# Kernel optimization log

Measured on AMD Instinct MI355X. Metric: run time of the kernel, lower is better.

Reference implementation:

```python
import jax, jax.numpy as jnp
import numpy as np
import math

B, T, C, H, RANK, RD = 8, 512, 2048, 16, 8, 16
HD = C // H  # 128
ADAPTER_SCALE = 1.0 / RANK  # scale / rank with scale=1.0


def setup_inputs() -> dict:
    key = jax.random.key(0)
    ks = jax.random.split(key, 7)
    x = jax.random.normal(ks[0], (B, T, C), dtype=jnp.float32)
    # frozen random linears (weights ~ N(0,1)/sqrt(in_features))
    Wqkv = jax.random.normal(ks[1], (3 * C, C), dtype=jnp.float32) / math.sqrt(C)
    Wout = jax.random.normal(ks[2], (C, C), dtype=jnp.float32) / math.sqrt(C)
    # VeRA frozen random matrices
    A0_qkv = jax.random.normal(ks[3], (RANK, C), dtype=jnp.float32) / math.sqrt(C)
    B0_qkv = jax.random.normal(ks[4], (3 * C, RANK), dtype=jnp.float32) / math.sqrt(RANK)
    A0_out = jax.random.normal(ks[5], (RANK, C), dtype=jnp.float32) / math.sqrt(C)
    B0_out = jax.random.normal(ks[6], (C, RANK), dtype=jnp.float32) / math.sqrt(RANK)
    # learned scaling vectors (init to ones, as in the module)
    d_a_qkv = jnp.ones((RANK,), dtype=jnp.float32)
    d_b_qkv = jnp.ones((RANK,), dtype=jnp.float32)
    d_a_out = jnp.ones((RANK,), dtype=jnp.float32)
    d_b_out = jnp.ones((RANK,), dtype=jnp.float32)
    # partial RoPE caches over first RD dims
    freqs = 1.0 / (10000.0 ** (jnp.arange(0, RD, 2, dtype=jnp.float32) / RD))  # [RD/2]
    ang = jnp.arange(T, dtype=jnp.float32)[:, None] * freqs[None, :]  # [T, RD/2]
    cos = jnp.cos(ang)
    sin = jnp.sin(ang)
    return {"x": x, "Wqkv": Wqkv, "A0_qkv": A0_qkv, "B0_qkv": B0_qkv,
            "d_a_qkv": d_a_qkv, "d_b_qkv": d_b_qkv,
            "Wout": Wout, "A0_out": A0_out, "B0_out": B0_out,
            "d_a_out": d_a_out, "d_b_out": d_b_out,
            "cos": cos, "sin": sin}


def _adapted_linear(x, W, A0, B0, d_a, d_b):
    # frozen(x) + VeRA adapter: diag(d_b) B0 diag(d_a) A0, scaled by 1/rank
    base = x @ W.T
    h = (x @ A0.T) * (d_a * d_b)
    return base + (h @ B0.T) * ADAPTER_SCALE


def _apply_rope(q, cos, sin):
    # q: [B, H, T, HD]; rotate first RD dims, pass-through the rest
    x_rope, x_pass = q[..., :RD], q[..., RD:]
    half = RD // 2
    x1, x2 = x_rope[..., :half], x_rope[..., half:]
    c = cos[None, None]  # [1,1,T,RD/2]
    s = sin[None, None]
    rot = jnp.concatenate([x1 * c - x2 * s, x2 * c + x1 * s], axis=-1)
    return jnp.concatenate([rot, x_pass], axis=-1)


def reference(x, Wqkv, A0_qkv, B0_qkv, d_a_qkv, d_b_qkv,
              Wout, A0_out, B0_out, d_a_out, d_b_out, cos, sin):
    qkv = _adapted_linear(x, Wqkv, A0_qkv, B0_qkv, d_a_qkv, d_b_qkv)  # [B,T,3C]
    qkv = qkv.reshape(B, T, 3, H, HD)
    q = jnp.transpose(qkv[:, :, 0], (0, 2, 1, 3))  # [B,H,T,HD]
    k = jnp.transpose(qkv[:, :, 1], (0, 2, 1, 3))
    v = jnp.transpose(qkv[:, :, 2], (0, 2, 1, 3))
    q = _apply_rope(q, cos, sin)
    k = _apply_rope(k, cos, sin)
    # causal SDPA
    scale = 1.0 / math.sqrt(HD)
    scores = jnp.einsum('bhqd,bhkd->bhqk', q, k) * scale
    mask = jnp.tril(jnp.ones((T, T), dtype=bool))
    scores = jnp.where(mask[None, None], scores, jnp.finfo(scores.dtype).min)
    attn = jax.nn.softmax(scores, axis=-1)
    y = jnp.einsum('bhqk,bhkd->bhqd', attn, v)  # [B,H,T,HD]
    y = jnp.transpose(y, (0, 2, 1, 3)).reshape(B, T, C)
    return _adapted_linear(y, Wout, A0_out, B0_out, d_a_out, d_b_out)
```

## Files before the change

### kernel.cpp

```cpp
#include <hip/hip_runtime.h>

typedef unsigned short ushort_t;
typedef __attribute__((ext_vector_type(8))) short short8;
typedef __attribute__((ext_vector_type(4))) float f32x4;

#define AS1(p) ((const __attribute__((address_space(1))) void*)(p))
#define AS3(p) ((__attribute__((address_space(3))) void*)(p))

__device__ __forceinline__ ushort_t f2bf(float f){
  unsigned u = __float_as_uint(f);
  u += 0x7FFFu + ((u>>16)&1u);
  return (ushort_t)(u>>16);
}
__device__ __forceinline__ float bf2f(ushort_t h){
  return __uint_as_float(((unsigned)h)<<16);
}

__global__ __launch_bounds__(256) void conv_f2b(const float* __restrict__ src,
                                                ushort_t* __restrict__ dst, int n){
  int i = (blockIdx.x*256 + threadIdx.x)*4;
  if (i < n){
    float4 v = *(const float4*)&src[i];
    ushort_t o0=f2bf(v.x), o1=f2bf(v.y), o2=f2bf(v.z), o3=f2bf(v.w);
    ushort4 o; o.x=o0; o.y=o1; o.z=o2; o.w=o3;
    *(ushort4*)&dst[i] = o;
  }
}

__global__ __launch_bounds__(256) void lora_h_f32(const float* __restrict__ X,
                                                  ushort_t* __restrict__ Xbf,
                                                  const float* __restrict__ A0,
                                                  const float* __restrict__ da,
                                                  const float* __restrict__ db,
                                                  float* __restrict__ out, int K){
  int m = blockIdx.x;
  int tid = threadIdx.x, lane = tid & 63, w = tid >> 6;
  float part[8] = {0,0,0,0,0,0,0,0};
  for (int k = tid; k < K; k += 256){
    float xv = X[(size_t)m*K + k];
    Xbf[(size_t)m*K + k] = f2bf(xv);
    #pragma unroll
    for (int r=0;r<8;++r) part[r] += xv * A0[r*K + k];
  }
  #pragma unroll
  for (int r=0;r<8;++r)
    for (int d=1;d<64;d<<=1) part[r] += __shfl_xor(part[r], d, 64);
  __shared__ float wsum[4][8];
  if (lane==0){
    #pragma unroll
    for (int r=0;r<8;++r) wsum[w][r] = part[r];
  }
  __syncthreads();
  if (tid < 8){
    float s = wsum[0][tid]+wsum[1][tid]+wsum[2][tid]+wsum[3][tid];
    out[(size_t)m*8 + tid] = s * da[tid]*db[tid];
  }
}

__global__ __launch_bounds__(256) void lora_reduce(const float* __restrict__ hpart,
                                                   const float* __restrict__ da,
                                                   const float* __restrict__ db,
                                                   float* __restrict__ out){
  int i = blockIdx.x*256 + threadIdx.x;
  int r = i & 7;
  float s = 0.f;
  #pragma unroll
  for (int hh=0; hh<16; ++hh) s += hpart[(size_t)hh*32768 + i];
  out[i] = s * da[r]*db[r];
}

__global__ __launch_bounds__(512, 1) void gemm256x192_lora(
    const ushort_t* __restrict__ A, const ushort_t* __restrict__ Bw,
    const float* __restrict__ hmat, const float* __restrict__ B0,
    ushort_t* __restrict__ C, int M, int N, int K)
{
  __shared__ __align__(16) char smem[114688];
  const int tid = threadIdx.x, lane = tid & 63, w = tid >> 6;
  const int wm = w >> 1, wn = w & 1;

  const int nbn = N / 192;
  const int nwg = (M >> 8) * nbn;
  const int q8 = nwg >> 3;
  const int swz = ((int)blockIdx.x & 7)*q8 + ((int)blockIdx.x >> 3);
  const int m0 = (swz / nbn) << 8, n0 = (swz % nbn) * 192;

  const int NTt = K >> 6;
  const int srow8  = tid >> 3;
  const int schunk = (lane & 7) ^ (lane >> 3);

  #define STAGE_AU(u, tt, bb) do { \
    const ushort_t* g_ = A + (size_t)(m0 + (u)*64 + srow8)*K + (tt)*64 + schunk*8; \
    __builtin_amdgcn_global_load_lds(AS1(g_), AS3(smem + (bb)*32768 + (u)*8192 + tid*16), 16, 0, 0); \
  } while(0)
  #define STAGE_BU(u, tt, bb) do { \
    const ushort_t* g_ = Bw + (size_t)(n0 + (u)*64 + srow8)*K + (tt)*64 + schunk*8; \
    __builtin_amdgcn_global_load_lds(AS1(g_), AS3(smem + 65536 + (bb)*24576 + (u)*8192 + tid*16), 16, 0, 0); \
  } while(0)

  #define RDA(bb, q, kk) (*(const short8*)(smem + (bb)*32768 + \
      ((q)*64 + wm*16 + (lane&15))*128 + ((((kk)*4 + (lane>>4)) ^ (lane&7))<<4)))
  #define RDB(bb, r, kk) (*(const short8*)(smem + 65536 + (bb)*24576 + \
      ((r)*32 + wn*16 + (lane&15))*128 + ((((kk)*4 + (lane>>4)) ^ (lane&7))<<4)))

  #define MM(q, r, bi) do{ \
    acc[q][r] = __builtin_amdgcn_mfma_f32_16x16x32_bf16(aF[q][0], bF[bi][0], acc[q][r], 0,0,0); \
    acc[q][r] = __builtin_amdgcn_mfma_f32_16x16x32_bf16(aF[q][1], bF[bi][1], acc[q][r], 0,0,0); \
  }while(0)

  #define BARRIER() asm volatile("s_barrier" ::: "memory")

  short8 aF[4][2];
  short8 bF[2][2];
  f32x4 acc[4][6] = {};

  STAGE_AU(0,0,0); STAGE_AU(1,0,0); STAGE_AU(2,0,0); STAGE_AU(3,0,0);
  STAGE_BU(0,0,0); STAGE_BU(1,0,0); STAGE_BU(2,0,0);
  asm volatile("s_waitcnt vmcnt(2)" ::: "memory");
  BARRIER();

  for (int t = 0; t < NTt-1; ++t){
    const int b = t & 1, nb = b ^ 1;
    #pragma unroll
    for (int q=0;q<4;++q){ aF[q][0]=RDA(b,q,0); aF[q][1]=RDA(b,q,1); }
    #pragma unroll
    for (int rl=0;rl<2;++rl){ bF[rl][0]=RDB(b,rl,0); bF[rl][1]=RDB(b,rl,1); }
    STAGE_AU(0,t+1,nb); STAGE_AU(1,t+1,nb);
    __builtin_amdgcn_s_setprio(1);
    MM(0,0,0); MM(0,1,1); MM(1,0,0); MM(1,1,1);
    MM(2,0,0); MM(2,1,1); MM(3,0,0); MM(3,1,1);
    __builtin_amdgcn_s_setprio(0);
    asm volatile("s_waitcnt vmcnt(3)" ::: "memory");
    BARRIER();
    #pragma unroll
    for (int rl=0;rl<2;++rl){ bF[rl][0]=RDB(b,rl+2,0); bF[rl][1]=RDB(b,rl+2,1); }
    STAGE_AU(2,t+1,nb); STAGE_AU(3,t+1,nb); STAGE_BU(0,t+1,nb);
    __builtin_amdgcn_s_setprio(1);
    MM(0,2,0); MM(0,3,1); MM(1,2,0); MM(1,3,1);
    MM(2,2,0); MM(2,3,1); MM(3,2,0); MM(3,3,1);
    __builtin_amdgcn_s_setprio(0);
    asm volatile("s_waitcnt vmcnt(5)" ::: "memory");
    BARRIER();
    #pragma unroll
    for (int rl=0;rl<2;++rl){ bF[rl][0]=RDB(b,rl+4,0); bF[rl][1]=RDB(b,rl+4,1); }
    STAGE_BU(1,t+1,nb); STAGE_BU(2,t+1,nb);
    __builtin_amdgcn_s_setprio(1);
    MM(0,4,0); MM(0,5,1); MM(1,4,0); MM(1,5,1);
    MM(2,4,0); MM(2,5,1); MM(3,4,0); MM(3,5,1);
    __builtin_amdgcn_s_setprio(0);
    asm volatile("s_waitcnt lgkmcnt(0)" ::: "memory");
    asm volatile("s_waitcnt vmcnt(2)" ::: "memory");
    BARRIER();
  }

  {
    const int b = (NTt-1) & 1;
    #pragma unroll
    for (int q=0;q<4;++q){ aF[q][0]=RDA(b,q,0); aF[q][1]=RDA(b,q,1); }
    #pragma unroll
    for (int rl=0;rl<2;++rl){ bF[rl][0]=RDB(b,rl,0); bF[rl][1]=RDB(b,rl,1); }
    __builtin_amdgcn_s_setprio(1);
    MM(0,0,0); MM(0,1,1); MM(1,0,0); MM(1,1,1);
    MM(2,0,0); MM(2,1,1); MM(3,0,0); MM(3,1,1);
    __builtin_amdgcn_s_setprio(0);
    asm volatile("s_waitcnt vmcnt(1)" ::: "memory");
    BARRIER();
    #pragma unroll
    for (int rl=0;rl<2;++rl){ bF[rl][0]=RDB(b,rl+2,0); bF[rl][1]=RDB(b,rl+2,1); }
    __builtin_amdgcn_s_setprio(1);
    MM(0,2,0); MM(0,3,1); MM(1,2,0); MM(1,3,1);
    MM(2,2,0); MM(2,3,1); MM(3,2,0); MM(3,3,1);
    __builtin_amdgcn_s_setprio(0);
    asm volatile("s_waitcnt vmcnt(0)" ::: "memory");
    BARRIER();
    #pragma unroll
    for (int rl=0;rl<2;++rl){ bF[rl][0]=RDB(b,rl+4,0); bF[rl][1]=RDB(b,rl+4,1); }
    MM(0,4,0); MM(0,5,1); MM(1,4,0); MM(1,5,1);
    MM(2,4,0); MM(2,5,1); MM(3,4,0); MM(3,5,1);
  }

  float b0v[6][8];
  #pragma unroll
  for (int r=0;r<6;++r){
    int col = n0 + r*32 + wn*16 + (lane&15);
    const float4* bp = (const float4*)&B0[(size_t)col*8];
    float4 u0 = bp[0], u1 = bp[1];
    b0v[r][0]=u0.x; b0v[r][1]=u0.y; b0v[r][2]=u0.z; b0v[r][3]=u0.w;
    b0v[r][4]=u1.x; b0v[r][5]=u1.y; b0v[r][6]=u1.z; b0v[r][7]=u1.w;
  }
  #pragma unroll
  for (int q=0;q<4;++q){
    #pragma unroll
    for (int jj=0;jj<4;++jj){
      int row = m0 + q*64 + wm*16 + (lane>>4)*4 + jj;
      const float4* hp = (const float4*)&hmat[(size_t)row*8];
      float4 h0 = hp[0], h1 = hp[1];
      #pragma unroll
      for (int r=0;r<6;++r){
        float lor = h0.x*b0v[r][0]+h0.y*b0v[r][1]+h0.z*b0v[r][2]+h0.w*b0v[r][3]
                  + h1.x*b0v[r][4]+h1.y*b0v[r][5]+h1.z*b0v[r][6]+h1.w*b0v[r][7];
        int col = n0 + r*32 + wn*16 + (lane&15);
        C[(size_t)row*N + col] = f2bf(acc[q][r][jj] + 0.125f*lor);
      }
    }
  }
  #undef STAGE_AU
  #undef STAGE_BU
  #undef RDA
  #undef RDB
  #undef MM
  #undef BARRIER
}

template<int MODE>
__global__ __launch_bounds__(512, 1) void gemm128x256_lora(
    const ushort_t* __restrict__ A, const ushort_t* __restrict__ Bw,
    const float* __restrict__ hmat, const float* __restrict__ B0,
    void* __restrict__ C, int M, int N, int K)
{
  __shared__ __align__(16) char smem[98304];
  const int tid = threadIdx.x, lane = tid & 63, w = tid >> 6;
  const int wm = w >> 2, wn = w & 3;

  const int nbn = N >> 8;
  const int nwg = (M >> 7) * nbn;
  const int q8 = nwg >> 3;
  const int swz = ((int)blockIdx.x & 7)*q8 + ((int)blockIdx.x >> 3);
  const int m0 = (swz / nbn) << 7, n0 = (swz % nbn) << 8;

  const int NTt = K >> 6;

  const int srow8  = tid >> 3;
  const int schunk = (lane & 7) ^ (lane >> 3);

  #define STAGE_AU(u, tt, bb) do { \
    const ushort_t* g_ = A + (size_t)(m0 + (u)*64 + srow8)*K + (tt)*64 + schunk*8; \
    __builtin_amdgcn_global_load_lds(AS1(g_), AS3(smem + (bb)*16384 + (u)*8192 + w*1024), 16, 0, 0); \
  } while(0)
  #define STAGE_BU(u, tt, bb) do { \
    const ushort_t* g_ = Bw + (size_t)(n0 + (u)*64 + srow8)*K + (tt)*64 + schunk*8; \
    __builtin_amdgcn_global_load_lds(AS1(g_), AS3(smem + 32768 + (bb)*32768 + (u)*8192 + w*1024), 16, 0, 0); \
  } while(0)

  #define RDA(bb, q, kk) (*(const short8*)(smem + (bb)*16384 + \
      ((q)*32 + wm*16 + (lane&15))*128 + ((((kk)*4 + (lane>>4)) ^ (lane&7))<<4)))
  #define RDB(bb, rg, kk) (*(const short8*)(smem + 32768 + (bb)*32768 + \
      ((rg)*64 + wn*16 + (lane&15))*128 + ((((kk)*4 + (lane>>4)) ^ (lane&7))<<4)))

  #define MM0(q,rl) do{ \
    acc[q][rl] = __builtin_amdgcn_mfma_f32_16x16x32_bf16(aF[q][0], bF[rl][0], acc[q][rl], 0,0,0); \
    acc[q][rl] = __builtin_amdgcn_mfma_f32_16x16x32_bf16(aF[q][1], bF[rl][1], acc[q][rl], 0,0,0); \
  }while(0)
  #define MM1(q,rl) do{ \
    acc[q][(rl)+2] = __builtin_amdgcn_mfma_f32_16x16x32_bf16(aF[q][0], bF[rl][0], acc[q][(rl)+2], 0,0,0); \
    acc[q][(rl)+2] = __builtin_amdgcn_mfma_f32_16x16x32_bf16(aF[q][1], bF[rl][1], acc[q][(rl)+2], 0,0,0); \
  }while(0)

  #define BARRIER() asm volatile("s_barrier" ::: "memory")

  short8 aF[4][2];
  short8 bF[2][2];
  f32x4 acc[4][4] = {};

  STAGE_AU(0,0,0); STAGE_AU(1,0,0); STAGE_BU(0,0,0); STAGE_BU(1,0,0);
  STAGE_BU(2,0,0); STAGE_BU(3,0,0);
  asm volatile("s_waitcnt vmcnt(2)" ::: "memory");
  BARRIER();

  for (int t = 0; t < NTt-1; ++t){
    const int b = t & 1, nb = b ^ 1;
    #pragma unroll
    for (int q=0;q<4;++q){ aF[q][0]=RDA(b,q,0); aF[q][1]=RDA(b,q,1); }
    #pragma unroll
    for (int rl=0;rl<2;++rl){ bF[rl][0]=RDB(b,rl,0); bF[rl][1]=RDB(b,rl,1); }
    STAGE_AU(0,t+1,nb); STAGE_AU(1,t+1,nb); STAGE_BU(0,t+1,nb); STAGE_BU(1,t+1,nb);
    __builtin_amdgcn_s_setprio(1);
    MM0(0,0); MM0(0,1); MM0(1,0); MM0(1,1);
    MM0(2,0); MM0(2,1); MM0(3,0); MM0(3,1);
    __builtin_amdgcn_s_setprio(0);
    asm volatile("s_waitcnt vmcnt(4)" ::: "memory");
    BARRIER();
    #pragma unroll
    for (int rl=0;rl<2;++rl){ bF[rl][0]=RDB(b,rl+2,0); bF[rl][1]=RDB(b,rl+2,1); }
    STAGE_BU(2,t+1,nb); STAGE_BU(3,t+1,nb);
    __builtin_amdgcn_s_setprio(1);
    MM1(0,0); MM1(0,1); MM1(1,0); MM1(1,1);
    MM1(2,0); MM1(2,1); MM1(3,0); MM1(3,1);
    __builtin_amdgcn_s_setprio(0);
    asm volatile("s_waitcnt lgkmcnt(0)" ::: "memory");
    asm volatile("s_waitcnt vmcnt(2)" ::: "memory");
    BARRIER();
  }

  {
    const int b = (NTt-1) & 1;
    #pragma unroll
    for (int q=0;q<4;++q){ aF[q][0]=RDA(b,q,0); aF[q][1]=RDA(b,q,1); }
    #pragma unroll
    for (int rl=0;rl<2;++rl){ bF[rl][0]=RDB(b,rl,0); bF[rl][1]=RDB(b,rl,1); }
    __builtin_amdgcn_s_setprio(1);
    MM0(0,0); MM0(0,1); MM0(1,0); MM0(1,1);
    MM0(2,0); MM0(2,1); MM0(3,0); MM0(3,1);
    __builtin_amdgcn_s_setprio(0);
    asm volatile("s_waitcnt vmcnt(0)" ::: "memory");
    BARRIER();
    #pragma unroll
    for (int rl=0;rl<2;++rl){ bF[rl][0]=RDB(b,rl+2,0); bF[rl][1]=RDB(b,rl+2,1); }
    MM1(0,0); MM1(0,1); MM1(1,0); MM1(1,1);
    MM1(2,0); MM1(2,1); MM1(3,0); MM1(3,1);
  }

  float b0v[4][8];
  #pragma unroll
  for (int r=0;r<4;++r){
    int col = n0 + r*64 + wn*16 + (lane&15);
    const float4* bp = (const float4*)&B0[(size_t)col*8];
    float4 u0 = bp[0], u1 = bp[1];
    b0v[r][0]=u0.x; b0v[r][1]=u0.y; b0v[r][2]=u0.z; b0v[r][3]=u0.w;
    b0v[r][4]=u1.x; b0v[r][5]=u1.y; b0v[r][6]=u1.z; b0v[r][7]=u1.w;
  }
  #pragma unroll
  for (int q=0;q<4;++q){
    #pragma unroll
    for (int jj=0;jj<4;++jj){
      int row = m0 + q*32 + wm*16 + (lane>>4)*4 + jj;
      const float4* hp = (const float4*)&hmat[(size_t)row*8];
      float4 h0 = hp[0], h1 = hp[1];
      #pragma unroll
      for (int r=0;r<4;++r){
        float lor = h0.x*b0v[r][0]+h0.y*b0v[r][1]+h0.z*b0v[r][2]+h0.w*b0v[r][3]
                  + h1.x*b0v[r][4]+h1.y*b0v[r][5]+h1.z*b0v[r][6]+h1.w*b0v[r][7];
        int col = n0 + r*64 + wn*16 + (lane&15);
        float v = acc[q][r][jj] + 0.125f*lor;
        if (MODE==0) ((ushort_t*)C)[(size_t)row*N + col] = f2bf(v);
        else         ((float*)C)[(size_t)row*N + col]    = v;
      }
    }
  }
  #undef STAGE_AU
  #undef STAGE_BU
  #undef RDA
  #undef RDB
  #undef MM0
  #undef MM1
  #undef BARRIER
}

__global__ __launch_bounds__(256) void rope_kernel(ushort_t* __restrict__ qkv,
                                                   const float* __restrict__ cosb,
                                                   const float* __restrict__ sinb){
  int idx = blockIdx.x*256 + threadIdx.x;
  int d = idx & 7;
  int g = idx >> 3;
  int h_ = g & 15;
  int s  = (g>>4) & 1;
  int t  = (g>>5) & 511;
  int b  = g >> 14;
  size_t base = (size_t)(b*512 + t)*6144 + s*2048 + h_*128;
  float x1 = bf2f(qkv[base+d]), x2 = bf2f(qkv[base+d+8]);
  float c = cosb[t*8+d], sn = sinb[t*8+d];
  qkv[base+d]   = f2bf(x1*c - x2*sn);
  qkv[base+d+8] = f2bf(x2*c + x1*sn);
}

__global__ __launch_bounds__(512) void attn_kernel(const ushort_t* __restrict__ qkv,
                                                   ushort_t* __restrict__ y,
                                                   const float* __restrict__ A0o,
                                                   float* __restrict__ hpart){
  __shared__ __align__(16) ushort_t Ks[2][64*128];
  __shared__ __align__(16) ushort_t Vt[2][128*64];
  __shared__ __align__(16) ushort_t Pl[8][16*64];

  const int flat = blockIdx.x;
  const int qt = ((flat >> 7) ^ ((flat >> 8) & 1)) & 3;
  const int hb = flat & 127;
  const int hh = hb & 15, b = hb >> 4;

  const int tid = threadIdx.x, lane = tid & 63, w = tid >> 6, g = lane >> 4;
  const int qb0 = qt*128;
  const int row_base = b*512;
  const int qoff = hh*128;
  const int koff = 2048 + hh*128;
  const int voff = 4096 + hh*128;
  const float scale = 0.08838834764831845f;

  short8 qf[4];
  {
    int qr = qb0 + w*16 + (lane & 15);
    const ushort_t* qp = qkv + (size_t)(row_base + qr)*6144 + qoff + g*8;
    #pragma unroll
    for (int kc=0;kc<4;++kc) qf[kc] = *(const short8*)(qp + kc*32);
  }

  const int krow = tid >> 4;
  const int kc_  = tid & 15;
  const int kcs  = (kc_ & 8) | ((kc_ ^ (krow & 7)) & 7);
  const int vr   = tid >> 3;
  const int vd0  = (tid & 7) * 16;
  const int vrhi = vr >> 3, vrlo = vr & 7;

  const int nt = 2*qt + 2;
  const int wmin = qb0 + w*16;
  const int wmax = wmin + 15;

  f32x4 o[8] = {};
  float mrow[4] = {-1e30f,-1e30f,-1e30f,-1e30f};
  float lrow[4] = {0,0,0,0};

  short8 vv0, vv1;

  {
    const ushort_t* kg = qkv + (size_t)(row_base + krow)*6144 + koff + kcs*8;
    __builtin_amdgcn_global_load_lds(AS1(kg), AS3((char*)&Ks[0][0] + tid*16), 16, 0, 0);
    __builtin_amdgcn_global_load_lds(AS1(kg + (size_t)32*6144), AS3((char*)&Ks[0][0] + 8192 + tid*16), 16, 0, 0);
    const ushort_t* vg = qkv + (size_t)(row_base + vr)*6144 + voff + vd0;
    vv0 = ((const short8*)vg)[0];
    vv1 = ((const short8*)vg)[1];
    #pragma unroll
    for (int ii=0;ii<8;++ii){
      int sw = (vrhi ^ ii) << 3;
      Vt[0][(vd0 + ii    )*64 + sw + vrlo] = (ushort_t)vv0[ii];
      Vt[0][(vd0 + 8 + ii)*64 + sw + vrlo] = (ushort_t)vv1[ii];
    }
  }
  __syncthreads();

  for (int t = 0; t < nt; ++t){
    const int bb = t & 1, nb = bb ^ 1;
    const int kv0 = t*64;
    const bool have_next = (t+1 < nt);

    if (have_next){
      const int kv1 = kv0 + 64;
      const ushort_t* kg = qkv + (size_t)(row_base + kv1 + krow)*6144 + koff + kcs*8;
      __builtin_amdgcn_global_load_lds(AS1(kg), AS3((char*)&Ks[nb][0] + tid*16), 16, 0, 0);
      __builtin_amdgcn_global_load_lds(AS1(kg + (size_t)32*6144), AS3((char*)&Ks[nb][0] + 8192 + tid*16), 16, 0, 0);
      const ushort_t* vg = qkv + (size_t)(row_base + kv1 + vr)*6144 + voff + vd0;
      vv0 = ((const short8*)vg)[0];
      vv1 = ((const short8*)vg)[1];
    }

    if (kv0 <= wmax){
      f32x4 s4[4] = {};
      #pragma unroll
      for (int cg=0;cg<4;++cg){
        const int row = cg*16 + (lane&15);
        const int rx = row & 7;
        #pragma unroll
        for (int kc=0;kc<4;++kc){
          const int ch = kc*4 + g;
          const short8 kfv = *(const short8*)&Ks[bb][row*128 + (((ch&8)|((ch^rx)&7))<<3)];
          s4[cg] = __builtin_amdgcn_mfma_f32_16x16x32_bf16(qf[kc], kfv, s4[cg], 0, 0, 0);
        }
      }

      const bool diag = (kv0 + 63 > wmin);
      float aa[4][4];
      float mx4[4];
      int needR = 0;
      #pragma unroll
      for (int j=0;j<4;++j){
        float a0 = s4[0][j]*scale, a1 = s4[1][j]*scale, a2 = s4[2][j]*scale, a3 = s4[3][j]*scale;
        if (diag){
          int q_abs = wmin + g*4 + j;
          int c0 = kv0 + (lane&15);
          if (c0      > q_abs) a0 = -1e30f;
          if (c0 + 16 > q_abs) a1 = -1e30f;
          if (c0 + 32 > q_abs) a2 = -1e30f;
          if (c0 + 48 > q_abs) a3 = -1e30f;
        }
        aa[j][0]=a0; aa[j][1]=a1; aa[j][2]=a2; aa[j][3]=a3;
        float mx = fmaxf(fmaxf(a0,a1), fmaxf(a2,a3));
        #pragma unroll
        for (int d=1; d<16; d<<=1) mx = fmaxf(mx, __shfl_xor(mx, d, 16));
        mx4[j] = mx;
        needR |= (mx > mrow[j] + 8.0f) ? 1 : 0;
      }
      needR = __any(needR);

      float p0[4], p1[4], p2[4], p3[4];
      if (needR){
        #pragma unroll
        for (int j=0;j<4;++j){
          float mn = fmaxf(mrow[j], mx4[j]);
          float f  = __expf(mrow[j] - mn);
          mrow[j] = mn;
          p0[j] = __expf(aa[j][0] - mn); p1[j] = __expf(aa[j][1] - mn);
          p2[j] = __expf(aa[j][2] - mn); p3[j] = __expf(aa[j][3] - mn);
          float rs = p0[j] + p1[j] + p2[j] + p3[j];
          #pragma unroll
          for (int d=1; d<16; d<<=1) rs += __shfl_xor(rs, d, 16);
          lrow[j] = lrow[j]*f + rs;
          #pragma unroll
          for (int n=0;n<8;++n) o[n][j] *= f;
        }
      } else {
        #pragma unroll
        for (int j=0;j<4;++j){
          p0[j] = __expf(aa[j][0] - mrow[j]); p1[j] = __expf(aa[j][1] - mrow[j]);
          p2[j] = __expf(aa[j][2] - mrow[j]); p3[j] = __expf(aa[j][3] - mrow[j]);
          float rs = p0[j] + p1[j] + p2[j] + p3[j];
          #pragma unroll
          for (int d=1; d<16; d<<=1) rs += __shfl_xor(rs, d, 16);
          lrow[j] += rs;
        }
      }

      {
        ushort_t* plw = &Pl[w][0];
        #pragma unroll
        for (int j=0;j<4;++j){
          const int prow = g*4 + j;
          const int rx = prow & 7;
          const int cl = (lane&15)>>3, c7 = lane&7;
          plw[prow*64 + (((0*2+cl)^rx)<<3) + c7] = f2bf(p0[j]);
          plw[prow*64 + (((1*2+cl)^rx)<<3) + c7] = f2bf(p1[j]);
          plw[prow*64 + (((2*2+cl)^rx)<<3) + c7] = f2bf(p2[j]);
          plw[prow*64 + (((3*2+cl)^rx)<<3) + c7] = f2bf(p3[j]);
        }
      }
      {
        const ushort_t* plw = &Pl[w][0];
        const int rowP = lane & 15, rxp = rowP & 7;
        const short8 pf0 = *(const short8*)&plw[rowP*64 + (((g  )^rxp)<<3)];
        const short8 pf1 = *(const short8*)&plw[rowP*64 + (((4+g)^rxp)<<3)];
        #pragma unroll
        for (int n=0;n<8;++n){
          const int d = n*16 + (lane&15);
          const int dx = d & 7;
          const short8 vf0 = *(const short8*)&Vt[bb][d*64 + (((g  )^dx)<<3)];
          const short8 vf1 = *(const short8*)&Vt[bb][d*64 + (((4+g)^dx)<<3)];
          o[n] = __builtin_amdgcn_mfma_f32_16x16x32_bf16(pf0, vf0, o[n], 0, 0, 0);
          o[n] = __builtin_amdgcn_mfma_f32_16x16x32_bf16(pf1, vf1, o[n], 0, 0, 0);
        }
      }
    }

    if (have_next){
      #pragma unroll
      for (int ii=0;ii<8;++ii){
        int sw = (vrhi ^ ii) << 3;
        Vt[nb][(vd0 + ii    )*64 + sw + vrlo] = (ushort_t)vv0[ii];
        Vt[nb][(vd0 + 8 + ii)*64 + sw + vrlo] = (ushort_t)vv1[ii];
      }
    }
    __syncthreads();
  }

  float invj[4];
  #pragma unroll
  for (int j=0;j<4;++j) invj[j] = 1.0f / lrow[j];

  #pragma unroll
  for (int j=0;j<4;++j){
    int qr = qb0 + w*16 + g*4 + j;
    #pragma unroll
    for (int n=0;n<8;++n)
      y[(size_t)(row_base+qr)*2048 + hh*128 + n*16 + (lane&15)] = f2bf(o[n][j]*invj[j]);
  }

  #pragma unroll
  for (int r=0;r<8;++r){
    float a0v[8];
    #pragma unroll
    for (int n=0;n<8;++n)
      a0v[n] = A0o[(size_t)r*2048 + hh*128 + n*16 + (lane&15)];
    #pragma unroll
    for (int j=0;j<4;++j){
      float s = 0.f;
      #pragma unroll
      for (int n=0;n<8;++n) s += o[n][j]*a0v[n];
      s *= invj[j];
      #pragma unroll
      for (int d=1; d<16; d<<=1) s += __shfl_xor(s, d, 16);
      if ((lane & 15) == 0){
        int qr = qb0 + w*16 + g*4 + j;
        hpart[((size_t)hh*4096 + row_base + qr)*8 + r] = s;
      }
    }
  }
}

extern "C" void kernel_launch(void* const* d_in, const int* in_sizes, int n_in,
                              void* d_out, int out_size, void* d_ws, size_t ws_size,
                              hipStream_t stream){
  const float* x       = (const float*)d_in[0];
  const float* Wqkv    = (const float*)d_in[1];
  const float* A0_qkv  = (const float*)d_in[2];
  const float* B0_qkv  = (const float*)d_in[3];
  const float* da_qkv  = (const float*)d_in[4];
  const float* db_qkv  = (const float*)d_in[5];
  const float* Wout    = (const float*)d_in[6];
  const float* A0_out  = (const float*)d_in[7];
  const float* B0_out  = (const float*)d_in[8];
  const float* da_out  = (const float*)d_in[9];
  const float* db_out  = (const float*)d_in[10];
  const float* cosb    = (const float*)d_in[11];
  const float* sinb    = (const float*)d_in[12];
  float* out = (float*)d_out;

  char* ws = (char*)d_ws;
  ushort_t* x_bf    = (ushort_t*)(ws);
  ushort_t* wqkv_bf = (ushort_t*)(ws + 16777216);
  ushort_t* wout_bf = (ushort_t*)(ws + 41943040);
  ushort_t* qkv_bf  = (ushort_t*)(ws + 50331648);
  ushort_t* y_bf    = (ushort_t*)(ws + 100663296);
  float*    h_qkv   = (float*)   (ws + 117440512);
  float*    h_out   = (float*)   (ws + 117571584);
  float*    h_part  = (float*)   (ws + 117702656);

  const int M = 4096;
  const int C = 2048;
  const int N3 = 6144;

  conv_f2b<<<12288,256, 0, stream>>>(Wqkv, wqkv_bf, N3*C);
  conv_f2b<<<4096, 256, 0, stream>>>(Wout, wout_bf, C*C);

  lora_h_f32<<<M, 256, 0, stream>>>(x, x_bf, A0_qkv, da_qkv, db_qkv, h_qkv, C);

  gemm256x192_lora<<<(M/256)*(N3/192), 512, 0, stream>>>(x_bf, wqkv_bf, h_qkv, B0_qkv,
                                                         qkv_bf, M, N3, C);

  rope_kernel<<<4096, 256, 0, stream>>>(qkv_bf, cosb, sinb);

  attn_kernel<<<512, 512, 0, stream>>>(qkv_bf, y_bf, A0_out, h_part);

  lora_reduce<<<128, 256, 0, stream>>>(h_part, da_out, db_out, h_out);

  gemm128x256_lora<1><<<(M/128)*(C/256), 512, 0, stream>>>(y_bf, wout_bf, h_out, B0_out,
                                                           out, M, C, C);
}
```

Baseline: 227.1 us.

## Shrink attention blocks to 64 query rows and drop K/V double buffering

```diff
diff --git a/kernel.cpp b/kernel.cpp
--- a/kernel.cpp
+++ b/kernel.cpp
@@ -362,21 +362,22 @@
   qkv[base+d+8] = f2bf(x2*c + x1*sn);
 }
 
-__global__ __launch_bounds__(512) void attn_kernel(const ushort_t* __restrict__ qkv,
+__global__ __launch_bounds__(256) void attn_kernel(const ushort_t* __restrict__ qkv,
                                                    ushort_t* __restrict__ y,
                                                    const float* __restrict__ A0o,
                                                    float* __restrict__ hpart){
-  __shared__ __align__(16) ushort_t Ks[2][64*128];
-  __shared__ __align__(16) ushort_t Vt[2][128*64];
-  __shared__ __align__(16) ushort_t Pl[8][16*64];
+  __shared__ __align__(16) ushort_t Ks[64*128];
+  __shared__ __align__(16) ushort_t Vt[128*64];
+  __shared__ __align__(16) ushort_t Pl[4][16*64];
 
   const int flat = blockIdx.x;
-  const int qt = ((flat >> 7) ^ ((flat >> 8) & 1)) & 3;
+  const int qsel = (flat >> 7) & 7;
+  const int qt = (0x54236710u >> (qsel*4)) & 7;
   const int hb = flat & 127;
   const int hh = hb & 15, b = hb >> 4;
 
   const int tid = threadIdx.x, lane = tid & 63, w = tid >> 6, g = lane >> 4;
-  const int qb0 = qt*128;
+  const int qb0 = qt*64;
   const int row_base = b*512;
   const int qoff = hh*128;
   const int koff = 2048 + hh*128;
@@ -394,156 +395,137 @@
   const int krow = tid >> 4;
   const int kc_  = tid & 15;
   const int kcs  = (kc_ & 8) | ((kc_ ^ (krow & 7)) & 7);
-  const int vr   = tid >> 3;
-  const int vd0  = (tid & 7) * 16;
+  const int vr   = tid >> 2;
+  const int vd0  = (tid & 3) * 32;
   const int vrhi = vr >> 3, vrlo = vr & 7;
 
-  const int nt = 2*qt + 2;
+  const int nt = qt + 1;
   const int wmin = qb0 + w*16;
-  const int wmax = wmin + 15;
 
   f32x4 o[8] = {};
   float mrow[4] = {-1e30f,-1e30f,-1e30f,-1e30f};
   float lrow[4] = {0,0,0,0};
 
-  short8 vv0, vv1;
-
-  {
-    const ushort_t* kg = qkv + (size_t)(row_base + krow)*6144 + koff + kcs*8;
-    __builtin_amdgcn_global_load_lds(AS1(kg), AS3((char*)&Ks[0][0] + tid*16), 16, 0, 0);
-    __builtin_amdgcn_global_load_lds(AS1(kg + (size_t)32*6144), AS3((char*)&Ks[0][0] + 8192 + tid*16), 16, 0, 0);
-    const ushort_t* vg = qkv + (size_t)(row_base + vr)*6144 + voff + vd0;
-    vv0 = ((const short8*)vg)[0];
-    vv1 = ((const short8*)vg)[1];
-    #pragma unroll
-    for (int ii=0;ii<8;++ii){
-      int sw = (vrhi ^ ii) << 3;
-      Vt[0][(vd0 + ii    )*64 + sw + vrlo] = (ushort_t)vv0[ii];
-      Vt[0][(vd0 + 8 + ii)*64 + sw + vrlo] = (ushort_t)vv1[ii];
-    }
-  }
-  __syncthreads();
-
   for (int t = 0; t < nt; ++t){
-    const int bb = t & 1, nb = bb ^ 1;
     const int kv0 = t*64;
-    const bool have_next = (t+1 < nt);
-
-    if (have_next){
-      const int kv1 = kv0 + 64;
-      const ushort_t* kg = qkv + (size_t)(row_base + kv1 + krow)*6144 + koff + kcs*8;
-      __builtin_amdgcn_global_load_lds(AS1(kg), AS3((char*)&Ks[nb][0] + tid*16), 16, 0, 0);
-      __builtin_amdgcn_global_load_lds(AS1(kg + (size_t)32*6144), AS3((char*)&Ks[nb][0] + 8192 + tid*16), 16, 0, 0);
-      const ushort_t* vg = qkv + (size_t)(row_base + kv1 + vr)*6144 + voff + vd0;
-      vv0 = ((const short8*)vg)[0];
-      vv1 = ((const short8*)vg)[1];
-    }
-
-    if (kv0 <= wmax){
-      f32x4 s4[4] = {};
-      #pragma unroll
-      for (int cg=0;cg<4;++cg){
-        const int row = cg*16 + (lane&15);
-        const int rx = row & 7;
-        #pragma unroll
-        for (int kc=0;kc<4;++kc){
-          const int ch = kc*4 + g;
-          const short8 kfv = *(const short8*)&Ks[bb][row*128 + (((ch&8)|((ch^rx)&7))<<3)];
-          s4[cg] = __builtin_amdgcn_mfma_f32_16x16x32_bf16(qf[kc], kfv, s4[cg], 0, 0, 0);
-        }
-      }
-
-      const bool diag = (kv0 + 63 > wmin);
-      float aa[4][4];
-      float mx4[4];
-      int needR = 0;
-      #pragma unroll
-      for (int j=0;j<4;++j){
-        float a0 = s4[0][j]*scale, a1 = s4[1][j]*scale, a2 = s4[2][j]*scale, a3 = s4[3][j]*scale;
-        if (diag){
-          int q_abs = wmin + g*4 + j;
-          int c0 = kv0 + (lane&15);
-          if (c0      > q_abs) a0 = -1e30f;
-          if (c0 + 16 > q_abs) a1 = -1e30f;
-          if (c0 + 32 > q_abs) a2 = -1e30f;
-          if (c0 + 48 > q_abs) a3 = -1e30f;
-        }
-        aa[j][0]=a0; aa[j][1]=a1; aa[j][2]=a2; aa[j][3]=a3;
-        float mx = fmaxf(fmaxf(a0,a1), fmaxf(a2,a3));
-        #pragma unroll
-        for (int d=1; d<16; d<<=1) mx = fmaxf(mx, __shfl_xor(mx, d, 16));
-        mx4[j] = mx;
-        needR |= (mx > mrow[j] + 8.0f) ? 1 : 0;
-      }
-      needR = __any(needR);
-
-      float p0[4], p1[4], p2[4], p3[4];
-      if (needR){
-        #pragma unroll
-        for (int j=0;j<4;++j){
-          float mn = fmaxf(mrow[j], mx4[j]);
-          float f  = __expf(mrow[j] - mn);
-          mrow[j] = mn;
-          p0[j] = __expf(aa[j][0] - mn); p1[j] = __expf(aa[j][1] - mn);
-          p2[j] = __expf(aa[j][2] - mn); p3[j] = __expf(aa[j][3] - mn);
-          float rs = p0[j] + p1[j] + p2[j] + p3[j];
-          #pragma unroll
-          for (int d=1; d<16; d<<=1) rs += __shfl_xor(rs, d, 16);
-          lrow[j] = lrow[j]*f + rs;
-          #pragma unroll
-          for (int n=0;n<8;++n) o[n][j] *= f;
-        }
-      } else {
-        #pragma unroll
-        for (int j=0;j<4;++j){
-          p0[j] = __expf(aa[j][0] - mrow[j]); p1[j] = __expf(aa[j][1] - mrow[j]);
-          p2[j] = __expf(aa[j][2] - mrow[j]); p3[j] = __expf(aa[j][3] - mrow[j]);
-          float rs = p0[j] + p1[j] + p2[j] + p3[j];
-          #pragma unroll
-          for (int d=1; d<16; d<<=1) rs += __shfl_xor(rs, d, 16);
-          lrow[j] += rs;
-        }
-      }
-
-      {
-        ushort_t* plw = &Pl[w][0];
-        #pragma unroll
-        for (int j=0;j<4;++j){
-          const int prow = g*4 + j;
-          const int rx = prow & 7;
-          const int cl = (lane&15)>>3, c7 = lane&7;
-          plw[prow*64 + (((0*2+cl)^rx)<<3) + c7] = f2bf(p0[j]);
-          plw[prow*64 + (((1*2+cl)^rx)<<3) + c7] = f2bf(p1[j]);
-          plw[prow*64 + (((2*2+cl)^rx)<<3) + c7] = f2bf(p2[j]);
-          plw[prow*64 + (((3*2+cl)^rx)<<3) + c7] = f2bf(p3[j]);
-        }
-      }
-      {
-        const ushort_t* plw = &Pl[w][0];
-        const int rowP = lane & 15, rxp = rowP & 7;
-        const short8 pf0 = *(const short8*)&plw[rowP*64 + (((g  )^rxp)<<3)];
-        const short8 pf1 = *(const short8*)&plw[rowP*64 + (((4+g)^rxp)<<3)];
-        #pragma unroll
-        for (int n=0;n<8;++n){
-          const int d = n*16 + (lane&15);
-          const int dx = d & 7;
-          const short8 vf0 = *(const short8*)&Vt[bb][d*64 + (((g  )^dx)<<3)];
-          const short8 vf1 = *(const short8*)&Vt[bb][d*64 + (((4+g)^dx)<<3)];
-          o[n] = __builtin_amdgcn_mfma_f32_16x16x32_bf16(pf0, vf0, o[n], 0, 0, 0);
-          o[n] = __builtin_amdgcn_mfma_f32_16x16x32_bf16(pf1, vf1, o[n], 0, 0, 0);
-        }
-      }
-    }
-
-    if (have_next){
+    __syncthreads();
+    {
+      const ushort_t* kg = qkv + (size_t)(row_base + kv0 + krow)*6144 + koff + kcs*8;
+      #pragma unroll
+      for (int i=0;i<4;++i)
+        __builtin_amdgcn_global_load_lds(AS1(kg + (size_t)(i*16)*6144),
+                                         AS3((char*)Ks + i*4096 + tid*16), 16, 0, 0);
+    }
+    {
+      const ushort_t* vg = qkv + (size_t)(row_base + kv0 + vr)*6144 + voff + vd0;
+      short8 vv0 = ((const short8*)vg)[0];
+      short8 vv1 = ((const short8*)vg)[1];
+      short8 vv2 = ((const short8*)vg)[2];
+      short8 vv3 = ((const short8*)vg)[3];
       #pragma unroll
       for (int ii=0;ii<8;++ii){
         int sw = (vrhi ^ ii) << 3;
-        Vt[nb][(vd0 + ii    )*64 + sw + vrlo] = (ushort_t)vv0[ii];
-        Vt[nb][(vd0 + 8 + ii)*64 + sw + vrlo] = (ushort_t)vv1[ii];
+        Vt[(vd0 + ii     )*64 + sw + vrlo] = (ushort_t)vv0[ii];
+        Vt[(vd0 + 8 + ii )*64 + sw + vrlo] = (ushort_t)vv1[ii];
+        Vt[(vd0 + 16 + ii)*64 + sw + vrlo] = (ushort_t)vv2[ii];
+        Vt[(vd0 + 24 + ii)*64 + sw + vrlo] = (ushort_t)vv3[ii];
       }
     }
     __syncthreads();
+
+    f32x4 s4[4] = {};
+    #pragma unroll
+    for (int cg=0;cg<4;++cg){
+      const int row = cg*16 + (lane&15);
+      const int rx = row & 7;
+      #pragma unroll
+      for (int kc=0;kc<4;++kc){
+        const int ch = kc*4 + g;
+        const short8 kfv = *(const short8*)&Ks[row*128 + (((ch&8)|((ch^rx)&7))<<3)];
+        s4[cg] = __builtin_amdgcn_mfma_f32_16x16x32_bf16(qf[kc], kfv, s4[cg], 0, 0, 0);
+      }
+    }
+
+    const bool diag = (kv0 + 63 > wmin);
+    float aa[4][4];
+    float mx4[4];
+    int needR = 0;
+    #pragma unroll
+    for (int j=0;j<4;++j){
+      float a0 = s4[0][j]*scale, a1 = s4[1][j]*scale, a2 = s4[2][j]*scale, a3 = s4[3][j]*scale;
+      if (diag){
+        int q_abs = wmin + g*4 + j;
+        int c0 = kv0 + (lane&15);
+        if (c0      > q_abs) a0 = -1e30f;
+        if (c0 + 16 > q_abs) a1 = -1e30f;
+        if (c0 + 32 > q_abs) a2 = -1e30f;
+        if (c0 + 48 > q_abs) a3 = -1e30f;
+      }
+      aa[j][0]=a0; aa[j][1]=a1; aa[j][2]=a2; aa[j][3]=a3;
+      float mx = fmaxf(fmaxf(a0,a1), fmaxf(a2,a3));
+      #pragma unroll
+      for (int d=1; d<16; d<<=1) mx = fmaxf(mx, __shfl_xor(mx, d, 16));
+      mx4[j] = mx;
+      needR |= (mx > mrow[j] + 8.0f) ? 1 : 0;
+    }
+    needR = __any(needR);
+
+    float p0[4], p1[4], p2[4], p3[4];
+    if (needR){
+      #pragma unroll
+      for (int j=0;j<4;++j){
+        float mn = fmaxf(mrow[j], mx4[j]);
+        float f  = __expf(mrow[j] - mn);
+        mrow[j] = mn;
+        p0[j] = __expf(aa[j][0] - mn); p1[j] = __expf(aa[j][1] - mn);
+        p2[j] = __expf(aa[j][2] - mn); p3[j] = __expf(aa[j][3] - mn);
+        float rs = p0[j] + p1[j] + p2[j] + p3[j];
+        #pragma unroll
+        for (int d=1; d<16; d<<=1) rs += __shfl_xor(rs, d, 16);
+        lrow[j] = lrow[j]*f + rs;
+        #pragma unroll
+        for (int n=0;n<8;++n) o[n][j] *= f;
+      }
+    } else {
+      #pragma unroll
+      for (int j=0;j<4;++j){
+        p0[j] = __expf(aa[j][0] - mrow[j]); p1[j] = __expf(aa[j][1] - mrow[j]);
+        p2[j] = __expf(aa[j][2] - mrow[j]); p3[j] = __expf(aa[j][3] - mrow[j]);
+        float rs = p0[j] + p1[j] + p2[j] + p3[j];
+        #pragma unroll
+        for (int d=1; d<16; d<<=1) rs += __shfl_xor(rs, d, 16);
+        lrow[j] += rs;
+      }
+    }
+
+    {
+      ushort_t* plw = &Pl[w][0];
+      #pragma unroll
+      for (int j=0;j<4;++j){
+        const int prow = g*4 + j;
+        const int rx = prow & 7;
+        const int cl = (lane&15)>>3, c7 = lane&7;
+        plw[prow*64 + (((0*2+cl)^rx)<<3) + c7] = f2bf(p0[j]);
+        plw[prow*64 + (((1*2+cl)^rx)<<3) + c7] = f2bf(p1[j]);
+        plw[prow*64 + (((2*2+cl)^rx)<<3) + c7] = f2bf(p2[j]);
+        plw[prow*64 + (((3*2+cl)^rx)<<3) + c7] = f2bf(p3[j]);
+      }
+    }
+    {
+      const ushort_t* plw = &Pl[w][0];
+      const int rowP = lane & 15, rxp = rowP & 7;
+      const short8 pf0 = *(const short8*)&plw[rowP*64 + (((g  )^rxp)<<3)];
+      const short8 pf1 = *(const short8*)&plw[rowP*64 + (((4+g)^rxp)<<3)];
+      #pragma unroll
+      for (int n=0;n<8;++n){
+        const int d = n*16 + (lane&15);
+        const int dx = d & 7;
+        const short8 vf0 = *(const short8*)&Vt[d*64 + (((g  )^dx)<<3)];
+        const short8 vf1 = *(const short8*)&Vt[d*64 + (((4+g)^dx)<<3)];
+        o[n] = __builtin_amdgcn_mfma_f32_16x16x32_bf16(pf0, vf0, o[n], 0, 0, 0);
+        o[n] = __builtin_amdgcn_mfma_f32_16x16x32_bf16(pf1, vf1, o[n], 0, 0, 0);
+      }
+    }
   }
 
   float invj[4];
@@ -622,7 +604,7 @@
 
   rope_kernel<<<4096, 256, 0, stream>>>(qkv_bf, cosb, sinb);
 
-  attn_kernel<<<512, 512, 0, stream>>>(qkv_bf, y_bf, A0_out, h_part);
+  attn_kernel<<<1024, 256, 0, stream>>>(qkv_bf, y_bf, A0_out, h_part);
 
   lora_reduce<<<128, 256, 0, stream>>>(h_part, da_out, db_out, h_out);
 
```

Result: slower. 236.3 us (+4.1%).
